# Performance work log

Measured on AMD Instinct MI355X. Metric: run time of the kernel, lower is better.

## Reference

```python
import jax, jax.numpy as jnp
import numpy as np

B, N, M, C, T, HF, WF = 4, 512, 32, 512, 8, 14, 14
K = 80          # num_classes
P = 7           # ROI pool output size
HID = 1024
IMG = 224


def setup_inputs() -> dict:
    key = jax.random.key(0)
    k0, k1, k2, k3, k4, k5 = jax.random.split(key, 6)
    feature = jax.random.normal(k0, (B, C, T, HF, WF), dtype=jnp.float32)
    # GT boxes: realistic xyxy boxes inside a 224x224 image
    ka, kb = jax.random.split(k1)
    cxy = jax.random.uniform(ka, (B, M, 2), minval=40.0, maxval=180.0)
    wh = jax.random.uniform(kb, (B, M, 2), minval=40.0, maxval=100.0)
    gt_bboxes = jnp.concatenate([cxy - wh / 2, cxy + wh / 2], axis=-1).astype(jnp.float32)
    # Proposals: jittered copies of GT boxes so many pass the IoU>=0.85 fg test
    idx = jnp.arange(N) % M
    base = gt_bboxes[:, idx]                                   # [B,N,4]
    noise = jax.random.normal(k2, (B, N, 4), dtype=jnp.float32) * 1.5
    proposal_bboxes = jnp.clip(base + noise, 0.0, float(IMG))
    gt_classes = (jax.random.uniform(k3, (B, M, K)) < 0.1).astype(jnp.float32)
    W1 = jax.random.normal(k4, (C * P * P, HID), dtype=jnp.float32) * 0.01
    b1 = jnp.zeros((HID,), jnp.float32)
    W2 = jax.random.normal(k5, (HID, K), dtype=jnp.float32) * 0.01
    b2 = jnp.zeros((K,), jnp.float32)
    return {"feature": feature, "proposal_bboxes": proposal_bboxes,
            "gt_bboxes": gt_bboxes, "gt_classes": gt_classes,
            "W1": W1, "b1": b1, "W2": W2, "b2": b2,
            "image_h": IMG, "image_w": IMG}


def _iou(a, b):
    # a [B,N,4], b [B,M,4] xyxy -> [B,N,M]
    lt = jnp.maximum(a[:, :, None, :2], b[:, None, :, :2])
    rb = jnp.minimum(a[:, :, None, 2:], b[:, None, :, 2:])
    wh = jnp.clip(rb - lt, 0.0)
    inter = wh[..., 0] * wh[..., 1]
    area_a = (a[..., 2] - a[..., 0]) * (a[..., 3] - a[..., 1])
    area_b = (b[..., 2] - b[..., 0]) * (b[..., 3] - b[..., 1])
    return inter / (area_a[:, :, None] + area_b[:, None, :] - inter + 1e-8)


def _roi_pool(feat_bhwc, boxes, bidx, sy, sx):
    # feat_bhwc [B,H,W,C]; boxes [R,4] image coords; bilinear 7x7 ROI pooling
    H, W = feat_bhwc.shape[1], feat_bhwc.shape[2]
    x1, y1, x2, y2 = boxes[:, 0] * sx, boxes[:, 1] * sy, boxes[:, 2] * sx, boxes[:, 3] * sy
    g = (jnp.arange(P, dtype=jnp.float32) + 0.5) / P
    ys = y1[:, None] + g[None, :] * (y2 - y1)[:, None]        # [R,P]
    xs = x1[:, None] + g[None, :] * (x2 - x1)[:, None]        # [R,P]
    y = jnp.broadcast_to(ys[:, :, None], (boxes.shape[0], P, P)) - 0.5
    x = jnp.broadcast_to(xs[:, None, :], (boxes.shape[0], P, P)) - 0.5
    y0f = jnp.floor(y); x0f = jnp.floor(x)
    wy = jnp.clip(y - y0f, 0.0, 1.0)[..., None]
    wx = jnp.clip(x - x0f, 0.0, 1.0)[..., None]
    y0 = jnp.clip(y0f, 0, H - 1).astype(jnp.int32)
    y1i = jnp.clip(y0f + 1, 0, H - 1).astype(jnp.int32)
    x0 = jnp.clip(x0f, 0, W - 1).astype(jnp.int32)
    x1i = jnp.clip(x0f + 1, 0, W - 1).astype(jnp.int32)
    bi = bidx[:, None, None]
    gather = lambda yy, xx: feat_bhwc[bi, yy, xx]             # [R,P,P,C]
    out = (gather(y0, x0) * (1 - wy) * (1 - wx) + gather(y0, x1i) * (1 - wy) * wx +
           gather(y1i, x0) * wy * (1 - wx) + gather(y1i, x1i) * wy * wx)
    return out


def reference(feature, proposal_bboxes, gt_bboxes, gt_classes, W1, b1, W2, b2, image_h, image_w):
    # temporal average pool (AvgPool3d over T) -> [B,C,HF,WF]
    feat = feature.mean(axis=2)
    feat_bhwc = jnp.transpose(feat, (0, 2, 3, 1))             # [B,HF,WF,C]
    # IoU-based fg assignment
    ious = _iou(proposal_bboxes, gt_bboxes)                   # [B,N,M]
    max_iou = ious.max(axis=2)                                # [B,N]
    assign = ious.argmax(axis=2)                              # [B,N]
    any_fg = jnp.any(max_iou >= 0.85)
    thresh = jnp.where(any_fg, 0.85, 0.5)                     # fallback branch
    fg = (max_iou >= thresh).astype(feature.dtype)            # [B,N]
    # ROI pool all proposals (bg masked out in the loss)
    boxes = proposal_bboxes.reshape(B * N, 4)
    bidx = jnp.repeat(jnp.arange(B, dtype=jnp.int32), N)
    sy = feat.shape[2] / float(image_h)
    sx = feat.shape[3] / float(image_w)
    pool = _roi_pool(feat_bhwc, boxes, bidx, sy, sx)          # [R,P,P,C]
    pool = jnp.transpose(pool, (0, 3, 1, 2)).reshape(B * N, C * P * P)
    hidden = jax.nn.relu(pool @ W1 + b1)                      # [R,HID]
    logits = hidden @ W2 + b2                                 # [R,K]
    # multilabel soft-margin labels per proposal
    labels = gt_classes[jnp.repeat(jnp.arange(B), N), assign.reshape(-1)]  # [R,K]
    per = -(labels * jax.nn.log_sigmoid(logits) +
            (1.0 - labels) * jax.nn.log_sigmoid(-logits)).mean(axis=-1)    # [R]
    per = per.reshape(B, N)
    cnt = fg.sum(axis=1)
    losses = jnp.where(cnt > 0, (per * fg).sum(axis=1) / jnp.maximum(cnt, 1.0), 0.0)
    return losses
```

## Files before the change

kernel.cpp:

```cpp
#include <hip/hip_runtime.h>
#include <cstdint>
#include <cstddef>

#define KTOT 25088
#define NBOX 2048
#define HID  1024

typedef __bf16 bf16x8 __attribute__((ext_vector_type(8)));
typedef float  f32x4  __attribute__((ext_vector_type(4)));

__device__ __forceinline__ unsigned short f2bf(float f) {
  union { float f; unsigned u; } v; v.f = f;
  unsigned r = v.u + 0x7FFFu + ((v.u >> 16) & 1u);
  return (unsigned short)(r >> 16);
}

__device__ __forceinline__ float scalar_f(const void* p) {
  int iv = *(const int*)p;
  if (iv > 0 && iv < (1 << 20)) return (float)iv;
  return *(const float*)p;
}

__global__ __launch_bounds__(256) void k_pre1(
    const float* __restrict__ W1, unsigned short* __restrict__ W1T,
    const float* __restrict__ feature, float* __restrict__ fbhwc,
    const float* __restrict__ prop, const float* __restrict__ gtb,
    float* __restrict__ max_iou, int* __restrict__ assign,
    int* __restrict__ flag) {
  __shared__ unsigned short tile[64][68];
  int blk = blockIdx.x;
  int t = threadIdx.x;
  if (blk < 6272) {
    int kp0 = (blk % 392) * 64;
    int h0  = (blk / 392) * 64;
    int seg = t & 15, ro = t >> 4;
#pragma unroll
    for (int r = 0; r < 4; ++r) {
      int i = ro + r * 16;
      int kp = kp0 + i;
      int srow = (kp & 511) * 49 + (kp >> 9);
      float4 v = *(const float4*)(W1 + (size_t)srow * 1024 + h0 + seg * 4);
      tile[i][seg*4+0] = f2bf(v.x);
      tile[i][seg*4+1] = f2bf(v.y);
      tile[i][seg*4+2] = f2bf(v.z);
      tile[i][seg*4+3] = f2bf(v.w);
    }
    __syncthreads();
#pragma unroll
    for (int r = 0; r < 4; ++r) {
      int hi = ro + r * 16;
      unsigned a = tile[seg*4+0][hi];
      unsigned b = tile[seg*4+1][hi];
      unsigned c = tile[seg*4+2][hi];
      unsigned d = tile[seg*4+3][hi];
      *(uint2*)(W1T + (size_t)(h0+hi)*KTOT + kp0 + seg*4) =
          make_uint2(a | (b << 16), c | (d << 16));
    }
  } else if (blk < 7840) {
    int id = (blk - 6272) * 256 + t;
    if (id >= 4 * 512 * 196) return;
    int pix = id % 196;
    int c   = (id / 196) & 511;
    int b   = id / (196 * 512);
    const float* p = feature + ((size_t)(b * 512 + c) * 8) * 196 + pix;
    float s = 0.f;
#pragma unroll
    for (int tt = 0; tt < 8; ++tt) s += p[tt * 196];
    fbhwc[((size_t)(b * 196 + pix)) * 512 + c] = s * 0.125f;
  } else {
    float* g = (float*)tile;
    int gid = (blk - 7840) * 256 + t;
    int b = gid >> 9;
    if (t < 128) g[t] = gtb[b * 128 + t];
    __syncthreads();
    float x1 = prop[gid * 4 + 0], y1 = prop[gid * 4 + 1];
    float x2 = prop[gid * 4 + 2], y2 = prop[gid * 4 + 3];
    float aa = (x2 - x1) * (y2 - y1);
    float best = -1e30f; int arg = 0;
    for (int m = 0; m < 32; ++m) {
      float gx1 = g[m*4], gy1 = g[m*4+1], gx2 = g[m*4+2], gy2 = g[m*4+3];
      float iw = fmaxf(fminf(x2, gx2) - fmaxf(x1, gx1), 0.f);
      float ih = fmaxf(fminf(y2, gy2) - fmaxf(y1, gy1), 0.f);
      float inter = iw * ih;
      float ab = (gx2 - gx1) * (gy2 - gy1);
      float iou = inter / (aa + ab - inter + 1e-8f);
      if (iou > best) { best = iou; arg = m; }
    }
    max_iou[gid] = best; assign[gid] = arg;
    if (best >= 0.85f) atomicOr(flag, 1);
  }
}

__global__ __launch_bounds__(256) void k_pre2(
    const float* __restrict__ fbhwc, const float* __restrict__ prop,
    const void* ihp, const void* iwp, unsigned short* __restrict__ Apool) {
  int blk = blockIdx.x;
  int t = threadIdx.x;
  int n = blk >> 1;
  int half = blk & 1;
  int start = half * 24;
  int end   = half ? 49 : 24;
  float sy = 14.f / scalar_f(ihp);
  float sx = 14.f / scalar_f(iwp);
  float bx1 = prop[n*4+0]*sx, by1 = prop[n*4+1]*sy;
  float bx2 = prop[n*4+2]*sx, by2 = prop[n*4+3]*sy;
  const float* fb = fbhwc + (size_t)(n >> 9) * 196 * 512;
  unsigned short* arow = Apool + (size_t)n * KTOT;
  int c4 = (t & 127) << 2;
  int bh = t >> 7;
  for (int b2i = start; b2i < end; b2i += 2) {
    int bin = b2i + bh;
    if (bin >= end) continue;
    int py = bin / 7, px = bin - py * 7;
    float y = by1 + ((py + 0.5f) * (1.f/7.f)) * (by2 - by1) - 0.5f;
    float x = bx1 + ((px + 0.5f) * (1.f/7.f)) * (bx2 - bx1) - 0.5f;
    float y0f = floorf(y), x0f = floorf(x);
    float wy = y - y0f, wx = x - x0f;
    int y0  = min(max((int)y0f, 0), 13);
    int y1i = min(max((int)y0f + 1, 0), 13);
    int x0  = min(max((int)x0f, 0), 13);
    int x1i = min(max((int)x0f + 1, 0), 13);
    float w00 = (1.f - wy) * (1.f - wx), w01 = (1.f - wy) * wx;
    float w10 = wy * (1.f - wx),         w11 = wy * wx;
    const float4 f00 = *(const float4*)(fb + (y0 * 14 + x0 ) * 512 + c4);
    const float4 f01 = *(const float4*)(fb + (y0 * 14 + x1i) * 512 + c4);
    const float4 f10 = *(const float4*)(fb + (y1i * 14 + x0 ) * 512 + c4);
    const float4 f11 = *(const float4*)(fb + (y1i * 14 + x1i) * 512 + c4);
    float vx = f00.x*w00 + f01.x*w01 + f10.x*w10 + f11.x*w11;
    float vy = f00.y*w00 + f01.y*w01 + f10.y*w10 + f11.y*w11;
    float vz = f00.z*w00 + f01.z*w01 + f10.z*w10 + f11.z*w11;
    float vw = f00.w*w00 + f01.w*w01 + f10.w*w10 + f11.w*w11;
    unsigned lo = (unsigned)f2bf(vx) | ((unsigned)f2bf(vy) << 16);
    unsigned hi = (unsigned)f2bf(vz) | ((unsigned)f2bf(vw) << 16);
    *(uint2*)(arow + bin * 512 + c4) = make_uint2(lo, hi);
  }
}

__device__ __forceinline__ void gload16(const unsigned short* g, unsigned short* l) {
  __builtin_amdgcn_global_load_lds(
      (const __attribute__((address_space(1))) unsigned int*)g,
      (__attribute__((address_space(3))) unsigned int*)l, 16, 0, 0);
}

__global__ __launch_bounds__(512, 2) void k_gemm1(
    const unsigned short* __restrict__ A,
    const unsigned short* __restrict__ B,
    unsigned short* __restrict__ hp)
{
  extern __shared__ unsigned short lds[];
  const int tid  = threadIdx.x;
  const int w    = tid >> 6;
  const int lane = tid & 63;
  const int l15  = lane & 15;
  const int wr = w >> 2, wc = w & 3;
  const int bid = (int)blockIdx.x;
  const int wg  = (bid & 7) * 32 + (bid >> 3);
  const int kb  = wg >> 5;
  const int gy  = (wg >> 2) & 7;
  const int gx  = wg & 3;

  f32x4 acc[8][4];
  const f32x4 zero = {0.f, 0.f, 0.f, 0.f};
#pragma unroll
  for (int m = 0; m < 8; ++m)
#pragma unroll
    for (int n = 0; n < 4; ++n) acc[m][n] = zero;

  const int xsw  = (tid & 7) ^ ((tid >> 3) & 7);
  const int rloc = ((tid >> 3) << 1) + (xsw >> 2);
  const int qsrc = xsw & 3;
  const size_t kbase = (size_t)kb * 3136;
  const unsigned short* gAp = A + (size_t)(gy * 256 + rloc) * KTOT + kbase + qsrc * 8;
  const unsigned short* gBp = B + (size_t)(gx * 256 + rloc) * KTOT + kbase + qsrc * 8;
  const int dstc = tid * 8;

  const int pfr   = ((lane >> 4) | ((l15 & 1) << 2)) ^ (l15 >> 1);
  const int aoffc = wr * 4096 + (l15 >> 1) * 64 + pfr * 8;
  const int boffc = wc * 2048 + (l15 >> 1) * 64 + pfr * 8;

  bf16x8 Afr[8], B0[4], B1[4];

#define STG(SLOT, KN) { \
    gload16(gAp + (KN),                      lds + (SLOT)*16384 + dstc); \
    gload16(gAp + (KN) + (size_t)128 * KTOT, lds + (SLOT)*16384 + 4096 + dstc); \
    gload16(gBp + (KN),                      lds + (SLOT)*16384 + 8192 + dstc); \
    gload16(gBp + (KN) + (size_t)128 * KTOT, lds + (SLOT)*16384 + 12288 + dstc); }
#define LDA(i, SLOT) Afr[i] = *reinterpret_cast<const bf16x8*>( \
    lds + (SLOT)*16384 + aoffc + (i)*512);
#define LDBx(arr, n, SLOT) arr[n] = *reinterpret_cast<const bf16x8*>( \
    lds + (SLOT)*16384 + 8192 + boffc + (n)*512);
#define VM4 asm volatile("s_waitcnt vmcnt(4)" ::: "memory");
#define VM0 asm volatile("s_waitcnt vmcnt(0)" ::: "memory");
#define VMN

#define STEP(BC, BN, CS, DOSTG, KN, VMASM, DOREFILL)                           \
  {                                                                            \
    if (DOSTG) STG((((CS)+2)&3), KN)                                           \
    VMASM                                                                      \
    __builtin_amdgcn_s_barrier();                                              \
    if (DOREFILL) { _Pragma("unroll") for (int n = 0; n < 4; ++n)              \
                      LDBx(BN, n, (((CS)+1)&3)) }                              \
    __builtin_amdgcn_s_setprio(1);                                             \
    _Pragma("unroll") for (int i = 0; i < 8; ++i) {                            \
      _Pragma("unroll") for (int n = 0; n < 4; ++n)                            \
        acc[i][n] = __builtin_amdgcn_mfma_f32_16x16x32_bf16(                   \
            Afr[i], BC[n], acc[i][n], 0, 0, 0);                                \
      if (DOREFILL) LDA(i, (((CS)+1)&3))                                       \
    }                                                                          \
    __builtin_amdgcn_s_setprio(0);                                             \
  }

  STG(0, 0)
  STG(1, 32)
  VM4
  __builtin_amdgcn_s_barrier();
#pragma unroll
  for (int i = 0; i < 8; ++i) LDA(i, 0)
#pragma unroll
  for (int n = 0; n < 4; ++n) LDBx(B0, n, 0)

#pragma unroll 1
  for (int s4 = 0; s4 < 96; s4 += 4) {
    STEP(B0, B1, 0, true, (size_t)(s4 + 2) * 32, VM4, true)
    STEP(B1, B0, 1, true, (size_t)(s4 + 3) * 32, VM4, true)
    STEP(B0, B1, 2, true, (size_t)(s4 + 4) * 32, VM4, true)
    STEP(B1, B0, 3, true, (size_t)(s4 + 5) * 32, VM4, true)
  }
  STEP(B0, B1, 0, false, 0, VM0, true)
  STEP(B1, B0, 1, false, 0, VMN, false)

#undef STEP
#undef VMN
#undef VM0
#undef VM4
#undef LDBx
#undef LDA
#undef STG

  unsigned short* o = hp + (size_t)kb * (2048u * 1024u);
  const int r0 = gy * 256 + wr * 128 + ((lane >> 4) << 2);
  const int c0 = gx * 256 + wc * 64 + l15;
#pragma unroll
  for (int m = 0; m < 8; ++m)
#pragma unroll
    for (int n = 0; n < 4; ++n)
#pragma unroll
      for (int j = 0; j < 4; ++j)
        o[(size_t)(r0 + m * 16 + j) * 1024 + c0 + n * 16] = f2bf(acc[m][n][j]);
}

template<int OUTBF>
__global__ __launch_bounds__(256, 4) void k_gemm(
    const unsigned short* __restrict__ A,
    const unsigned short* __restrict__ B,
    void* __restrict__ outp,
    int Kst, int kIters, int nTileBits, int mTileBits, int ldc)
{
  __shared__ unsigned short As[2][4096];
  __shared__ unsigned short Bs[2][4096];
  const int tid  = threadIdx.x;
  const int w    = tid >> 6;
  const int lane = tid & 63;
  const int nwg = (int)gridDim.x, cpx = nwg >> 3;
  const int bid = (int)blockIdx.x;
  const int wg  = (bid & 7) * cpx + (bid >> 3);
  const int kb  = wg >> (mTileBits + nTileBits);
  const int rem = wg & ((1 << (mTileBits + nTileBits)) - 1);
  const int gy  = rem >> nTileBits;
  const int gx  = rem & ((1 << nTileBits) - 1);
  const int wr = w >> 1, wc = w & 1;

  f32x4 acc[4][4];
  const f32x4 zero = {0.f, 0.f, 0.f, 0.f};
#pragma unroll
  for (int m = 0; m < 4; ++m)
#pragma unroll
    for (int n = 0; n < 4; ++n) acc[m][n] = zero;

  const int r0   = 32 * w + (lane >> 2);
  const int qsrc = (lane & 3) ^ ((lane >> 3) & 3);
  const size_t kbase = (size_t)kb * kIters * 32;
  const unsigned short* gA = A + (size_t)(gy * 128 + r0) * Kst + kbase + qsrc * 8;
  const unsigned short* gB = B + (size_t)(gx * 128 + r0) * Kst + kbase + qsrc * 8;
  const int ldst = r0 * 32 + (lane & 3) * 8;

  const int swq = ((lane >> 4) ^ ((lane >> 1) & 3)) * 8;
  const int ar = (wr * 64 + (lane & 15)) * 32 + swq;
  const int br = (wc * 64 + (lane & 15)) * 32 + swq;

#define STAGE(bufi, it) do {                                         \
    const unsigned short* pa = gA + (size_t)(it) * 32;               \
    const unsigned short* pb = gB + (size_t)(it) * 32;               \
    gload16(pa,                      &As[bufi][ldst]);               \
    gload16(pa + (size_t)16 * Kst,   &As[bufi][ldst + 512]);         \
    gload16(pb,                      &Bs[bufi][ldst]);               \
    gload16(pb + (size_t)16 * Kst,   &Bs[bufi][ldst + 512]);         \
  } while (0)

  STAGE(0, 0);
  int cur = 0;
  for (int kk = 0; kk < kIters; ++kk) {
    __syncthreads();
    if (kk + 1 < kIters) STAGE(cur ^ 1, kk + 1);
    bf16x8 af[4], bfr[4];
#pragma unroll
    for (int m = 0; m < 4; ++m)
      af[m] = *reinterpret_cast<const bf16x8*>(&As[cur][ar + m * 512]);
#pragma unroll
    for (int n = 0; n < 4; ++n)
      bfr[n] = *reinterpret_cast<const bf16x8*>(&Bs[cur][br + n * 512]);
#pragma unroll
    for (int m = 0; m < 4; ++m)
#pragma unroll
      for (int n = 0; n < 4; ++n)
        acc[m][n] = __builtin_amdgcn_mfma_f32_16x16x32_bf16(af[m], bfr[n], acc[m][n], 0, 0, 0);
    cur ^= 1;
  }
#undef STAGE

  const size_t M = (size_t)(1 << mTileBits) * 128;
  const size_t splitStride = M * (size_t)ldc;
  const int r0o = gy * 128 + wr * 64 + ((lane >> 4) << 2);
  const int c0o = gx * 128 + wc * 64 + (lane & 15);
  if (OUTBF) {
    unsigned short* o = (unsigned short*)outp + (size_t)kb * splitStride;
#pragma unroll
    for (int m = 0; m < 4; ++m)
#pragma unroll
      for (int n = 0; n < 4; ++n)
#pragma unroll
        for (int j = 0; j < 4; ++j)
          o[(size_t)(r0o + m * 16 + j) * ldc + c0o + n * 16] = f2bf(acc[m][n][j]);
  } else {
    float* o = (float*)outp + (size_t)kb * splitStride;
#pragma unroll
    for (int m = 0; m < 4; ++m)
#pragma unroll
      for (int n = 0; n < 4; ++n)
#pragma unroll
        for (int j = 0; j < 4; ++j)
          o[(size_t)(r0o + m * 16 + j) * ldc + c0o + n * 16] = acc[m][n][j];
  }
}

__global__ __launch_bounds__(256) void k_combine(const unsigned short* __restrict__ hp,
                                                 const float* __restrict__ b1,
                                                 unsigned short* __restrict__ hidden,
                                                 const float* __restrict__ W2,
                                                 unsigned short* __restrict__ W2T) {
  int blk = blockIdx.x;
  if (blk >= 1024) {
    int id = (blk - 1024) * 256 + threadIdx.x;
    int cls = id >> 10, k = id & 1023;
    float v = (cls < 80) ? W2[(size_t)k * 80 + cls] : 0.f;
    W2T[id] = f2bf(v);
    return;
  }
  int gid = blk * 256 + threadIdx.x;
  int id8 = gid * 8;
  int h = id8 & 1023;
  float a[8];
#pragma unroll
  for (int j = 0; j < 8; ++j) a[j] = b1[h + j];
#pragma unroll
  for (int s = 0; s < 8; ++s) {
    uint4 u = *(const uint4*)(hp + (size_t)s * 2097152 + id8);
    unsigned uu[4] = {u.x, u.y, u.z, u.w};
#pragma unroll
    for (int q = 0; q < 4; ++q) {
      union { unsigned u; float f; } lo, hi;
      lo.u = uu[q] << 16; hi.u = uu[q] & 0xFFFF0000u;
      a[2*q]   += lo.f;
      a[2*q+1] += hi.f;
    }
  }
  unsigned out[4];
#pragma unroll
  for (int q = 0; q < 4; ++q) {
    unsigned l  = f2bf(fmaxf(a[2*q],   0.f));
    unsigned hh = f2bf(fmaxf(a[2*q+1], 0.f));
    out[q] = l | (hh << 16);
  }
  *(uint4*)(hidden + id8) = make_uint4(out[0], out[1], out[2], out[3]);
}

__global__ __launch_bounds__(256) void k_bce(const float* __restrict__ hp2,
                                             const float* __restrict__ b2,
                                             const float* __restrict__ gtc,
                                             const int* __restrict__ assign,
                                             float* __restrict__ per) {
  __shared__ float red[256];
  int t = threadIdx.x;
  int box = t >> 4, li = t & 15;
  int n = blockIdx.x * 16 + box;
  int lab = ((n >> 9) * 32 + assign[n]) * 80;
  float s = 0.f;
#pragma unroll
  for (int j = 0; j < 5; ++j) {
    int c = li + 16 * j;
    size_t o = (size_t)n * 128 + c;
    float x = b2[c];
#pragma unroll
    for (int sp = 0; sp < 8; ++sp) x += hp2[o + (size_t)sp * 262144];
    float y = gtc[lab + c];
    float ce = log1pf(expf(-fabsf(x)));
    s += y * (fmaxf(-x, 0.f) + ce) + (1.f - y) * (fmaxf(x, 0.f) + ce);
  }
  red[t] = s;
  __syncthreads();
  if (li == 0) {
    float tot = 0.f;
#pragma unroll
    for (int i = 0; i < 16; ++i) tot += red[box * 16 + i];
    per[n] = tot * (1.f / 80.f);
  }
}

__global__ __launch_bounds__(512) void k_reduce(const float* __restrict__ per,
                                                const float* __restrict__ max_iou,
                                                const int* __restrict__ flag,
                                                float* __restrict__ out) {
  __shared__ float sv[8], sf[8];
  int b = blockIdx.x, tid = threadIdx.x;
  float thr = (*flag) ? 0.85f : 0.5f;
  int n = b * 512 + tid;
  float f = (max_iou[n] >= thr) ? 1.f : 0.f;
  float v = per[n] * f;
#pragma unroll
  for (int o = 32; o > 0; o >>= 1) {
    v += __shfl_down(v, o);
    f += __shfl_down(f, o);
  }
  int wv = tid >> 6;
  if ((tid & 63) == 0) { sv[wv] = v; sf[wv] = f; }
  __syncthreads();
  if (tid == 0) {
    float S = 0.f, F = 0.f;
#pragma unroll
    for (int i = 0; i < 8; ++i) { S += sv[i]; F += sf[i]; }
    out[b] = (F > 0.f) ? S / fmaxf(F, 1.f) : 0.f;
  }
}

extern "C" void kernel_launch(void* const* d_in, const int* in_sizes, int n_in,
                              void* d_out, int out_size, void* d_ws, size_t ws_size,
                              hipStream_t stream) {
  const float* feature = (const float*)d_in[0];
  const float* prop    = (const float*)d_in[1];
  const float* gtb     = (const float*)d_in[2];
  const float* gtc     = (const float*)d_in[3];
  const float* W1      = (const float*)d_in[4];
  const float* b1      = (const float*)d_in[5];
  const float* W2      = (const float*)d_in[6];
  const float* b2      = (const float*)d_in[7];
  const void*  ihp     = d_in[8];
  const void*  iwp     = d_in[9];

  char* ws = (char*)d_ws;
  float*          fbhwc  = (float*)(ws);
  unsigned short* W1T    = (unsigned short*)(ws + 1605632);
  unsigned short* Apool  = (unsigned short*)(ws + 52985856);
  unsigned short* hp     = (unsigned short*)(ws + 155746304);
  float*          max_iou= (float*)(ws + 189300736);
  int*            assign = (int*)(ws + 189308928);
  float*          per    = (float*)(ws + 189317120);
  int*            flag   = (int*)(ws + 189325312);
  unsigned short* hidden = W1T;
  unsigned short* W2T    = Apool;
  float*          hp2    = (float*)((char*)Apool + 262144);

  hipFuncSetAttribute((const void*)k_gemm1,
                      hipFuncAttributeMaxDynamicSharedMemorySize, 131072);

  hipMemsetAsync(flag, 0, sizeof(int), stream);
  k_pre1   <<<7848, 256, 0, stream>>>(W1, W1T, feature, fbhwc, prop, gtb,
                                      max_iou, assign, flag);
  k_pre2   <<<4096, 256, 0, stream>>>(fbhwc, prop, ihp, iwp, Apool);
  k_gemm1  <<<256, 512, 131072, stream>>>(Apool, W1T, hp);
  k_combine<<<1536, 256, 0, stream>>>(hp, b1, hidden, W2, W2T);
  k_gemm<0><<<128, 256, 0, stream>>>(hidden, W2T, hp2, 1024, 4, 0, 4, 128);
  k_bce    <<<128, 256, 0, stream>>>(hp2, b2, gtc, assign, per);
  k_reduce <<<4, 512, 0, stream>>>(per, max_iou, flag, (float*)d_out);
}
```

Before: 186.0 us.

## Quantize ROI-pool activations and W1 to FP8 for the large GEMM

Converts the pooled activations and transposed W1 from bf16 to FP8 (e4m3 with software rounding). W1 is pre-scaled by 64 and the scale is undone in the combine step. The main GEMM switches to fp8 MFMA, with LDS layout, offsets and K-step count reworked for one-byte elements, which halves the bytes moved through global memory and LDS. This trades numerical accuracy for bandwidth and MFMA throughput, and risks tolerance failures from FP8 rounding of both operands.

```diff
diff --git a/kernel.cpp b/kernel.cpp
--- a/kernel.cpp
+++ b/kernel.cpp
@@ -15,6 +15,26 @@
   return (unsigned short)(r >> 16);
 }
 
+__device__ __forceinline__ unsigned char f2fp8(float x) {
+  union { float f; unsigned u; } v; v.f = x;
+  unsigned sign = (v.u >> 31) << 7;
+  float a = fabsf(x);
+  if (!(a >= 0.001953125f)) {
+    int q = (int)rintf(a * 512.f);
+    return (unsigned char)(sign | q);
+  }
+  if (a >= 464.f) return (unsigned char)(sign | 0x7E);
+  int e = (int)((v.u >> 23) & 0xFF) - 127;
+  if (e < -6) {
+    int q = (int)rintf(ldexpf(a, 9));
+    return (unsigned char)(sign | q);
+  }
+  int q = (int)rintf(ldexpf(a, 3 - e));
+  if (q == 16) { e += 1; q = 8; }
+  if (e > 8) return (unsigned char)(sign | 0x7E);
+  return (unsigned char)(sign | ((e + 7) << 3) | (q - 8));
+}
+
 __device__ __forceinline__ float scalar_f(const void* p) {
   int iv = *(const int*)p;
   if (iv > 0 && iv < (1 << 20)) return (float)iv;
@@ -22,12 +42,12 @@
 }
 
 __global__ __launch_bounds__(256) void k_pre1(
-    const float* __restrict__ W1, unsigned short* __restrict__ W1T,
+    const float* __restrict__ W1, unsigned char* __restrict__ W1T,
     const float* __restrict__ feature, float* __restrict__ fbhwc,
     const float* __restrict__ prop, const float* __restrict__ gtb,
     float* __restrict__ max_iou, int* __restrict__ assign,
     int* __restrict__ flag) {
-  __shared__ unsigned short tile[64][68];
+  __shared__ unsigned char tile[64][68];
   int blk = blockIdx.x;
   int t = threadIdx.x;
   if (blk < 6272) {
@@ -40,10 +60,10 @@
       int kp = kp0 + i;
       int srow = (kp & 511) * 49 + (kp >> 9);
       float4 v = *(const float4*)(W1 + (size_t)srow * 1024 + h0 + seg * 4);
-      tile[i][seg*4+0] = f2bf(v.x);
-      tile[i][seg*4+1] = f2bf(v.y);
-      tile[i][seg*4+2] = f2bf(v.z);
-      tile[i][seg*4+3] = f2bf(v.w);
+      tile[i][seg*4+0] = f2fp8(v.x * 64.f);
+      tile[i][seg*4+1] = f2fp8(v.y * 64.f);
+      tile[i][seg*4+2] = f2fp8(v.z * 64.f);
+      tile[i][seg*4+3] = f2fp8(v.w * 64.f);
     }
     __syncthreads();
 #pragma unroll
@@ -53,8 +73,8 @@
       unsigned b = tile[seg*4+1][hi];
       unsigned c = tile[seg*4+2][hi];
       unsigned d = tile[seg*4+3][hi];
-      *(uint2*)(W1T + (size_t)(h0+hi)*KTOT + kp0 + seg*4) =
-          make_uint2(a | (b << 16), c | (d << 16));
+      *(unsigned*)(W1T + (size_t)(h0+hi)*KTOT + kp0 + seg*4) =
+          a | (b << 8) | (c << 16) | (d << 24);
     }
   } else if (blk < 7840) {
     int id = (blk - 6272) * 256 + t;
@@ -93,7 +113,7 @@
 
 __global__ __launch_bounds__(256) void k_pre2(
     const float* __restrict__ fbhwc, const float* __restrict__ prop,
-    const void* ihp, const void* iwp, unsigned short* __restrict__ Apool) {
+    const void* ihp, const void* iwp, unsigned char* __restrict__ Apool) {
   int blk = blockIdx.x;
   int t = threadIdx.x;
   int n = blk >> 1;
@@ -105,7 +125,7 @@
   float bx1 = prop[n*4+0]*sx, by1 = prop[n*4+1]*sy;
   float bx2 = prop[n*4+2]*sx, by2 = prop[n*4+3]*sy;
   const float* fb = fbhwc + (size_t)(n >> 9) * 196 * 512;
-  unsigned short* arow = Apool + (size_t)n * KTOT;
+  unsigned char* arow = Apool + (size_t)n * KTOT;
   int c4 = (t & 127) << 2;
   int bh = t >> 7;
   for (int b2i = start; b2i < end; b2i += 2) {
@@ -130,24 +150,24 @@
     float vy = f00.y*w00 + f01.y*w01 + f10.y*w10 + f11.y*w11;
     float vz = f00.z*w00 + f01.z*w01 + f10.z*w10 + f11.z*w11;
     float vw = f00.w*w00 + f01.w*w01 + f10.w*w10 + f11.w*w11;
-    unsigned lo = (unsigned)f2bf(vx) | ((unsigned)f2bf(vy) << 16);
-    unsigned hi = (unsigned)f2bf(vz) | ((unsigned)f2bf(vw) << 16);
-    *(uint2*)(arow + bin * 512 + c4) = make_uint2(lo, hi);
-  }
-}
-
-__device__ __forceinline__ void gload16(const unsigned short* g, unsigned short* l) {
+    unsigned pk = (unsigned)f2fp8(vx) | ((unsigned)f2fp8(vy) << 8)
+                | ((unsigned)f2fp8(vz) << 16) | ((unsigned)f2fp8(vw) << 24);
+    *(unsigned*)(arow + bin * 512 + c4) = pk;
+  }
+}
+
+__device__ __forceinline__ void gload16(const unsigned char* g, unsigned char* l) {
   __builtin_amdgcn_global_load_lds(
       (const __attribute__((address_space(1))) unsigned int*)g,
       (__attribute__((address_space(3))) unsigned int*)l, 16, 0, 0);
 }
 
 __global__ __launch_bounds__(512, 2) void k_gemm1(
-    const unsigned short* __restrict__ A,
-    const unsigned short* __restrict__ B,
+    const unsigned char* __restrict__ A,
+    const unsigned char* __restrict__ B,
     unsigned short* __restrict__ hp)
 {
-  extern __shared__ unsigned short lds[];
+  extern __shared__ unsigned char lds[];
   const int tid  = threadIdx.x;
   const int w    = tid >> 6;
   const int lane = tid & 63;
@@ -170,70 +190,86 @@
   const int rloc = ((tid >> 3) << 1) + (xsw >> 2);
   const int qsrc = xsw & 3;
   const size_t kbase = (size_t)kb * 3136;
-  const unsigned short* gAp = A + (size_t)(gy * 256 + rloc) * KTOT + kbase + qsrc * 8;
-  const unsigned short* gBp = B + (size_t)(gx * 256 + rloc) * KTOT + kbase + qsrc * 8;
-  const int dstc = tid * 8;
-
-  const int pfr   = ((lane >> 4) | ((l15 & 1) << 2)) ^ (l15 >> 1);
-  const int aoffc = wr * 4096 + (l15 >> 1) * 64 + pfr * 8;
-  const int boffc = wc * 2048 + (l15 >> 1) * 64 + pfr * 8;
-
-  bf16x8 Afr[8], B0[4], B1[4];
+  const unsigned char* gAp = A + (size_t)(gy * 256 + rloc) * KTOT + kbase + qsrc * 16;
+  const unsigned char* gBp = B + (size_t)(gx * 256 + rloc) * KTOT + kbase + qsrc * 16;
+  const int dstc = tid * 16;
+
+  const int g4   = lane >> 4;
+  const int qb   = g4 >> 1;
+  const int h8   = (g4 & 1) * 8;
+  const int rpar = (l15 & 1) << 2;
+  const int lin  = l15 >> 1;
+  const int P0 = ((qb)     | rpar) ^ lin;
+  const int P1 = ((qb + 2) | rpar) ^ lin;
+  const int aoff0 = wr * 8192 + lin * 128 + P0 * 16 + h8;
+  const int aoff1 = wr * 8192 + lin * 128 + P1 * 16 + h8;
+  const int boff0 = 16384 + wc * 4096 + lin * 128 + P0 * 16 + h8;
+  const int boff1 = 16384 + wc * 4096 + lin * 128 + P1 * 16 + h8;
+
+  long A0[8], A1[8], Bk0[4], Bk1[4];
 
 #define STG(SLOT, KN) { \
-    gload16(gAp + (KN),                      lds + (SLOT)*16384 + dstc); \
-    gload16(gAp + (KN) + (size_t)128 * KTOT, lds + (SLOT)*16384 + 4096 + dstc); \
-    gload16(gBp + (KN),                      lds + (SLOT)*16384 + 8192 + dstc); \
-    gload16(gBp + (KN) + (size_t)128 * KTOT, lds + (SLOT)*16384 + 12288 + dstc); }
-#define LDA(i, SLOT) Afr[i] = *reinterpret_cast<const bf16x8*>( \
-    lds + (SLOT)*16384 + aoffc + (i)*512);
-#define LDBx(arr, n, SLOT) arr[n] = *reinterpret_cast<const bf16x8*>( \
-    lds + (SLOT)*16384 + 8192 + boffc + (n)*512);
+    gload16(gAp + (KN),                      lds + (SLOT)*32768 + dstc); \
+    gload16(gAp + (KN) + (size_t)128 * KTOT, lds + (SLOT)*32768 + 8192 + dstc); \
+    gload16(gBp + (KN),                      lds + (SLOT)*32768 + 16384 + dstc); \
+    gload16(gBp + (KN) + (size_t)128 * KTOT, lds + (SLOT)*32768 + 24576 + dstc); }
+#define LDA(m, SLOT) { \
+    A0[m] = *(const long*)(lds + (SLOT)*32768 + aoff0 + (m)*1024); \
+    A1[m] = *(const long*)(lds + (SLOT)*32768 + aoff1 + (m)*1024); }
+#define LDB(n, SLOT) { \
+    Bk0[n] = *(const long*)(lds + (SLOT)*32768 + boff0 + (n)*1024); \
+    Bk1[n] = *(const long*)(lds + (SLOT)*32768 + boff1 + (n)*1024); }
 #define VM4 asm volatile("s_waitcnt vmcnt(4)" ::: "memory");
 #define VM0 asm volatile("s_waitcnt vmcnt(0)" ::: "memory");
 #define VMN
 
-#define STEP(BC, BN, CS, DOSTG, KN, VMASM, DOREFILL)                           \
+#define STEP(CS, DOSTG, KN, VMASM, DOREFILL)                                   \
   {                                                                            \
     if (DOSTG) STG((((CS)+2)&3), KN)                                           \
     VMASM                                                                      \
     __builtin_amdgcn_s_barrier();                                              \
+    __builtin_amdgcn_s_setprio(1);                                             \
+    _Pragma("unroll") for (int m = 0; m < 8; ++m) {                            \
+      _Pragma("unroll") for (int n = 0; n < 4; ++n) {                          \
+        acc[m][n] = __builtin_amdgcn_mfma_f32_16x16x32_fp8_fp8(                \
+            A0[m], Bk0[n], acc[m][n], 0, 0, 0);                                \
+        acc[m][n] = __builtin_amdgcn_mfma_f32_16x16x32_fp8_fp8(                \
+            A1[m], Bk1[n], acc[m][n], 0, 0, 0);                                \
+      }                                                                        \
+      if (DOREFILL) LDA(m, (((CS)+1)&3))                                       \
+    }                                                                          \
     if (DOREFILL) { _Pragma("unroll") for (int n = 0; n < 4; ++n)              \
-                      LDBx(BN, n, (((CS)+1)&3)) }                              \
-    __builtin_amdgcn_s_setprio(1);                                             \
-    _Pragma("unroll") for (int i = 0; i < 8; ++i) {                            \
-      _Pragma("unroll") for (int n = 0; n < 4; ++n)                            \
-        acc[i][n] = __builtin_amdgcn_mfma_f32_16x16x32_bf16(                   \
-            Afr[i], BC[n], acc[i][n], 0, 0, 0);                                \
-      if (DOREFILL) LDA(i, (((CS)+1)&3))                                       \
-    }                                                                          \
+                      LDB(n, (((CS)+1)&3)) }                                   \
     __builtin_amdgcn_s_setprio(0);                                             \
   }
 
   STG(0, 0)
-  STG(1, 32)
+  STG(1, 64)
   VM4
   __builtin_amdgcn_s_barrier();
 #pragma unroll
-  for (int i = 0; i < 8; ++i) LDA(i, 0)
-#pragma unroll
-  for (int n = 0; n < 4; ++n) LDBx(B0, n, 0)
+  for (int m = 0; m < 8; ++m) LDA(m, 0)
+#pragma unroll
+  for (int n = 0; n < 4; ++n) LDB(n, 0)
 
 #pragma unroll 1
-  for (int s4 = 0; s4 < 96; s4 += 4) {
-    STEP(B0, B1, 0, true, (size_t)(s4 + 2) * 32, VM4, true)
-    STEP(B1, B0, 1, true, (size_t)(s4 + 3) * 32, VM4, true)
-    STEP(B0, B1, 2, true, (size_t)(s4 + 4) * 32, VM4, true)
-    STEP(B1, B0, 3, true, (size_t)(s4 + 5) * 32, VM4, true)
-  }
-  STEP(B0, B1, 0, false, 0, VM0, true)
-  STEP(B1, B0, 1, false, 0, VMN, false)
+  for (int s4 = 0; s4 < 44; s4 += 4) {
+    STEP(0, true, (size_t)(s4 + 2) * 64, VM4, true)
+    STEP(1, true, (size_t)(s4 + 3) * 64, VM4, true)
+    STEP(2, true, (size_t)(s4 + 4) * 64, VM4, true)
+    STEP(3, true, (size_t)(s4 + 5) * 64, VM4, true)
+  }
+  STEP(0, true, (size_t)46 * 64, VM4, true)
+  STEP(1, true, (size_t)47 * 64, VM4, true)
+  STEP(2, true, (size_t)48 * 64, VM4, true)
+  STEP(3, false, 0, VM0, true)
+  STEP(0, false, 0, VMN, false)
 
 #undef STEP
 #undef VMN
 #undef VM0
 #undef VM4
-#undef LDBx
+#undef LDB
 #undef LDA
 #undef STG
 
@@ -247,6 +283,12 @@
 #pragma unroll
       for (int j = 0; j < 4; ++j)
         o[(size_t)(r0 + m * 16 + j) * 1024 + c0 + n * 16] = f2bf(acc[m][n][j]);
+}
+
+__device__ __forceinline__ void gload16s(const unsigned short* g, unsigned short* l) {
+  __builtin_amdgcn_global_load_lds(
+      (const __attribute__((address_space(1))) unsigned int*)g,
+      (__attribute__((address_space(3))) unsigned int*)l, 16, 0, 0);
 }
 
 template<int OUTBF>
@@ -291,10 +333,10 @@
 #define STAGE(bufi, it) do {                                         \
     const unsigned short* pa = gA + (size_t)(it) * 32;               \
     const unsigned short* pb = gB + (size_t)(it) * 32;               \
-    gload16(pa,                      &As[bufi][ldst]);               \
-    gload16(pa + (size_t)16 * Kst,   &As[bufi][ldst + 512]);         \
-    gload16(pb,                      &Bs[bufi][ldst]);               \
-    gload16(pb + (size_t)16 * Kst,   &Bs[bufi][ldst + 512]);         \
+    gload16s(pa,                      &As[bufi][ldst]);              \
+    gload16s(pa + (size_t)16 * Kst,   &As[bufi][ldst + 512]);        \
+    gload16s(pb,                      &Bs[bufi][ldst]);              \
+    gload16s(pb + (size_t)16 * Kst,   &Bs[bufi][ldst + 512]);        \
   } while (0)
 
   STAGE(0, 0);
@@ -359,9 +401,7 @@
   int gid = blk * 256 + threadIdx.x;
   int id8 = gid * 8;
   int h = id8 & 1023;
-  float a[8];
-#pragma unroll
-  for (int j = 0; j < 8; ++j) a[j] = b1[h + j];
+  float a[8] = {0.f, 0.f, 0.f, 0.f, 0.f, 0.f, 0.f, 0.f};
 #pragma unroll
   for (int s = 0; s < 8; ++s) {
     uint4 u = *(const uint4*)(hp + (size_t)s * 2097152 + id8);
@@ -377,8 +417,10 @@
   unsigned out[4];
 #pragma unroll
   for (int q = 0; q < 4; ++q) {
-    unsigned l  = f2bf(fmaxf(a[2*q],   0.f));
-    unsigned hh = f2bf(fmaxf(a[2*q+1], 0.f));
+    float v0 = a[2*q]   * 0.015625f + b1[h + 2*q];
+    float v1 = a[2*q+1] * 0.015625f + b1[h + 2*q + 1];
+    unsigned l  = f2bf(fmaxf(v0, 0.f));
+    unsigned hh = f2bf(fmaxf(v1, 0.f));
     out[q] = l | (hh << 16);
   }
   *(uint4*)(hidden + id8) = make_uint4(out[0], out[1], out[2], out[3]);
@@ -458,15 +500,15 @@
 
   char* ws = (char*)d_ws;
   float*          fbhwc  = (float*)(ws);
-  unsigned short* W1T    = (unsigned short*)(ws + 1605632);
-  unsigned short* Apool  = (unsigned short*)(ws + 52985856);
+  unsigned char*  W1T    = (unsigned char*)(ws + 1605632);
+  unsigned char*  Apool  = (unsigned char*)(ws + 52985856);
   unsigned short* hp     = (unsigned short*)(ws + 155746304);
   float*          max_iou= (float*)(ws + 189300736);
   int*            assign = (int*)(ws + 189308928);
   float*          per    = (float*)(ws + 189317120);
   int*            flag   = (int*)(ws + 189325312);
-  unsigned short* hidden = W1T;
-  unsigned short* W2T    = Apool;
+  unsigned short* hidden = (unsigned short*)W1T;
+  unsigned short* W2T    = (unsigned short*)Apool;
   float*          hp2    = (float*)((char*)Apool + 262144);
 
   hipFuncSetAttribute((const void*)k_gemm1,
```

After: 179.0 us. 1.04x faster.
